# Performance work log

Measured on AMD Instinct MI355X. Metric: run time of the kernel, lower is better.

Reference implementation:

```python
import jax, jax.numpy as jnp
import numpy as np

NUM_EXPERTS = 8
TOP_K = 2
D_MODEL = 1024
D_MLP = 3584
BATCH, POS = 2, 2048


def setup_inputs() -> dict:
    key = jax.random.key(0)
    ks = jax.random.split(key, 5)
    scale = 0.02
    x = jax.random.normal(ks[0], (BATCH, POS, D_MODEL), dtype=jnp.float32)
    W_gate = jax.random.normal(ks[1], (NUM_EXPERTS, D_MODEL), dtype=jnp.float32) * scale
    W1 = jax.random.normal(ks[2], (NUM_EXPERTS, D_MLP, D_MODEL), dtype=jnp.float32) * scale
    W3 = jax.random.normal(ks[3], (NUM_EXPERTS, D_MLP, D_MODEL), dtype=jnp.float32) * scale
    W2 = jax.random.normal(ks[4], (NUM_EXPERTS, D_MODEL, D_MLP), dtype=jnp.float32) * scale
    return {"x": x, "W_gate": W_gate, "W1": W1, "W3": W3, "W2": W2}


def reference(x, W_gate, W1, W3, W2):
    batch, pos, d_model = x.shape
    xt = x.reshape(-1, d_model)                      # [T, d]
    T = xt.shape[0]

    # --- top-2 softmax gating ---
    gate_logits = xt @ W_gate.T                      # [T, E]
    weights = jax.nn.softmax(gate_logits.astype(jnp.float32), axis=-1)
    top_w, top_i = jax.lax.top_k(weights, TOP_K)     # [T, k]
    top_w = top_w / jnp.sum(top_w, axis=-1, keepdims=True)
    top_w = top_w.astype(gate_logits.dtype)

    # dense combine weights: zero for non-selected experts  [T, E]
    combine = jnp.zeros((T, NUM_EXPERTS), dtype=xt.dtype)
    combine = combine.at[jnp.arange(T)[:, None], top_i].set(top_w)

    # --- per-expert SwiGLU MLP, computed dense over all tokens ---
    h1 = jnp.einsum('td,efd->etf', xt, W1)           # [E, T, ffn]
    h3 = jnp.einsum('td,efd->etf', xt, W3)           # [E, T, ffn]
    h = jax.nn.silu(h1) * h3                         # [E, T, ffn]
    expert_out = jnp.einsum('etf,edf->etd', h, W2)   # [E, T, d]

    # --- weighted combine ---
    out = jnp.einsum('etd,te->td', expert_out, combine)  # [T, d]
    return out.reshape(batch, pos, d_model)
```

## Files before the change

kernel.cpp:

```cpp
#include <hip/hip_runtime.h>
#include <hip/hip_bf16.h>
#include <math.h>


#define NUM_EXPERTS 8
#define TOPK 2
#define D_MODEL 1024
#define D_MLP 3584
#define T_TOKENS 4096
#define NSLOT (T_TOKENS * TOPK)
#define SLOT_CAP 9216

#define BM 128
#define BN 128
#define BK 32
#define LDT 40

typedef __attribute__((ext_vector_type(8))) short bf16x8;
typedef __attribute__((ext_vector_type(4))) float f32x4;

#define WS_SMALL 147456
#define H_BYTES ((size_t)SLOT_CAP * D_MLP * 2)
#define XB_OFF (WS_SMALL + H_BYTES)
#define XB_BYTES ((size_t)T_TOKENS * D_MODEL * 2)
#define W1B_OFF (XB_OFF + XB_BYTES)
#define W13_BYTES ((size_t)NUM_EXPERTS * (size_t)D_MLP * D_MODEL * 2)
#define W3B_OFF (W1B_OFF + W13_BYTES)
#define WS_FULL (W3B_OFF + W13_BYTES)
#define WS_NEEDED_OLD (WS_SMALL + H_BYTES)

__device__ inline unsigned short f32_to_bf16(float f) {
  union { float f; unsigned int u; } v; v.f = f;
  unsigned int u = v.u;
  unsigned int r = (u + 0x7FFFu + ((u >> 16) & 1u)) >> 16;
  return (unsigned short)r;
}

__device__ inline bf16x8 pack8(float4 a, float4 b) {
  bf16x8 v;
  v[0] = (short)f32_to_bf16(a.x); v[1] = (short)f32_to_bf16(a.y);
  v[2] = (short)f32_to_bf16(a.z); v[3] = (short)f32_to_bf16(a.w);
  v[4] = (short)f32_to_bf16(b.x); v[5] = (short)f32_to_bf16(b.y);
  v[6] = (short)f32_to_bf16(b.z); v[7] = (short)f32_to_bf16(b.w);
  return v;
}

__device__ __forceinline__ void gload16(const void* g, void* l) {
  __builtin_amdgcn_global_load_lds(
      (__attribute__((address_space(1))) void*)g,
      (__attribute__((address_space(3))) void*)l, 16, 0, 0);
}

__global__ void zero_kernel(float4* __restrict__ p, int n4) {
  int i = blockIdx.x * blockDim.x + threadIdx.x;
  if (i < n4) p[i] = make_float4(0.f, 0.f, 0.f, 0.f);
}

__global__ __launch_bounds__(256) void cvt_kernel(const float* __restrict__ src,
                                                  unsigned short* __restrict__ dst,
                                                  int n8) {
  int i = blockIdx.x * blockDim.x + threadIdx.x;
  const int stride = gridDim.x * blockDim.x;
  for (; i < n8; i += stride) {
    const float4* s = (const float4*)(src + (size_t)i * 8);
    float4 a = s[0], b = s[1];
    *(bf16x8*)(dst + (size_t)i * 8) = pack8(a, b);
  }
}

__global__ __launch_bounds__(64) void gate_kernel(const float* __restrict__ x,
                            const float* __restrict__ Wg,
                            int* __restrict__ top_idx,
                            float* __restrict__ top_w) {
  const int t = blockIdx.x;
  const int lane = threadIdx.x;
  const float* xr = x + (size_t)t * D_MODEL;

  float xs[16];
#pragma unroll
  for (int i = 0; i < 16; ++i) xs[i] = xr[lane + i * 64];

  float logits[NUM_EXPERTS];
#pragma unroll
  for (int e = 0; e < NUM_EXPERTS; ++e) {
    const float* wr = Wg + (size_t)e * D_MODEL;
    float s = 0.f;
#pragma unroll
    for (int i = 0; i < 16; ++i) s += xs[i] * wr[lane + i * 64];
    for (int o = 32; o > 0; o >>= 1) s += __shfl_down(s, o);
    logits[e] = s;
  }

  if (lane == 0) {
    int i0 = 0;
#pragma unroll
    for (int e = 1; e < NUM_EXPERTS; ++e)
      if (logits[e] > logits[i0]) i0 = e;
    int i1 = -1;
#pragma unroll
    for (int e = 0; e < NUM_EXPERTS; ++e) {
      if (e == i0) continue;
      if (i1 < 0 || logits[e] > logits[i1]) i1 = e;
    }
    float w0 = 1.0f / (1.0f + expf(logits[i1] - logits[i0]));
    top_idx[2 * t] = i0; top_idx[2 * t + 1] = i1;
    top_w[2 * t] = w0;   top_w[2 * t + 1] = 1.0f - w0;
  }
}

__global__ __launch_bounds__(256) void route_kernel(int* __restrict__ top_idx,
                             const float* __restrict__ top_w,
                             int* __restrict__ hdr,
                             int* __restrict__ slot_token,
                             float* __restrict__ slot_weight) {
  __shared__ int cnt[NUM_EXPERTS];
  __shared__ int off[NUM_EXPERTS];
  __shared__ int cur[NUM_EXPERTS];
  const int tid = threadIdx.x;
  if (tid < NUM_EXPERTS) cnt[tid] = 0;
  __syncthreads();
  for (int k = tid; k < NSLOT; k += 256) atomicAdd(&cnt[top_idx[k]], 1);
  __syncthreads();
  if (tid == 0) {
    int o = 0;
    for (int e = 0; e < NUM_EXPERTS; ++e) {
      off[e] = o;
      int p = (cnt[e] + BM - 1) & ~(BM - 1);
      hdr[e] = cnt[e];
      hdr[8 + e] = o;
      hdr[16 + e] = p;
      o += p;
    }
  }
  __syncthreads();
  if (tid < NUM_EXPERTS) cur[tid] = off[tid];
  for (int i = tid; i < SLOT_CAP; i += 256) { slot_token[i] = 0; slot_weight[i] = 0.0f; }
  __syncthreads();
  for (int k = tid; k < NSLOT; k += 256) {
    int e = top_idx[k];
    int p = atomicAdd(&cur[e], 1);
    slot_token[p] = k >> 1;
    slot_weight[p] = top_w[k];
    top_idx[k] = p;
  }
}

__global__ __launch_bounds__(256) void gemm1_p(
    const unsigned short* __restrict__ Xb,
    const unsigned short* __restrict__ W1b,
    const unsigned short* __restrict__ W3b,
    const int* __restrict__ hdr,
    const int* __restrict__ slot_token,
    unsigned short* __restrict__ H) {
  const int e = blockIdx.z;
  const int pad_cnt = hdr[16 + e];
  const int m0 = blockIdx.y * BM;
  if (m0 >= pad_cnt) return;
  const int base = hdr[8 + e];
  const int n0 = blockIdx.x * BN;

  __shared__ unsigned short As[2][BM * BK];
  __shared__ unsigned short B1s[2][BN * BK];
  __shared__ unsigned short B3s[2][BN * BK];

  const int tid = threadIdx.x;
  const int lane = tid & 63;
  const int wave = tid >> 6;
  const int wm = (wave >> 1) * 64;
  const int wn = (wave & 1) * 64;
  const int l15 = lane & 15;
  const int quad = lane >> 4;

  const int r0 = tid >> 2;
  const int cc = (tid & 3) * 8;
  const int tokA0 = slot_token[base + m0 + r0];
  const int tokA1 = slot_token[base + m0 + 64 + r0];
  const unsigned short* gA0 = Xb + (size_t)tokA0 * D_MODEL + cc;
  const unsigned short* gA1 = Xb + (size_t)tokA1 * D_MODEL + cc;
  const unsigned short* gB1_0 = W1b + ((size_t)e * D_MLP + n0 + r0) * D_MODEL + cc;
  const unsigned short* gB1_1 = gB1_0 + (size_t)64 * D_MODEL;
  const unsigned short* gB3_0 = W3b + ((size_t)e * D_MLP + n0 + r0) * D_MODEL + cc;
  const unsigned short* gB3_1 = gB3_0 + (size_t)64 * D_MODEL;
  const int wb = wave * 512;

  const f32x4 fzero = {0.f, 0.f, 0.f, 0.f};
  f32x4 acc1[4][4], acc3[4][4];
#pragma unroll
  for (int i = 0; i < 4; ++i)
#pragma unroll
    for (int j = 0; j < 4; ++j) { acc1[i][j] = fzero; acc3[i][j] = fzero; }

#define NT1 (D_MODEL / BK)
  {
    gload16(gA0, &As[0][wb]);
    gload16(gA1, &As[0][2048 + wb]);
    gload16(gB1_0, &B1s[0][wb]);
    gload16(gB1_1, &B1s[0][2048 + wb]);
    gload16(gB3_0, &B3s[0][wb]);
    gload16(gB3_1, &B3s[0][2048 + wb]);
  }
  __syncthreads();

#pragma unroll
  for (int t = 0; t < NT1; ++t) {
    const int p = t & 1;
    if (t + 1 < NT1) {
      const int q = (t + 1) & 1;
      const int k1 = (t + 1) * BK;
      gload16(gA0 + k1, &As[q][wb]);
      gload16(gA1 + k1, &As[q][2048 + wb]);
      gload16(gB1_0 + k1, &B1s[q][wb]);
      gload16(gB1_1 + k1, &B1s[q][2048 + wb]);
      gload16(gB3_0 + k1, &B3s[q][wb]);
      gload16(gB3_1 + k1, &B3s[q][2048 + wb]);
    }
    bf16x8 af[4], b1f[4], b3f[4];
#pragma unroll
    for (int i = 0; i < 4; ++i)
      af[i] = *(const bf16x8*)(&As[p][(wm + i * 16 + l15) * BK + quad * 8]);
#pragma unroll
    for (int j = 0; j < 4; ++j) {
      b1f[j] = *(const bf16x8*)(&B1s[p][(wn + j * 16 + l15) * BK + quad * 8]);
      b3f[j] = *(const bf16x8*)(&B3s[p][(wn + j * 16 + l15) * BK + quad * 8]);
    }
#pragma unroll
    for (int i = 0; i < 4; ++i)
#pragma unroll
      for (int j = 0; j < 4; ++j) {
        acc1[i][j] = __builtin_amdgcn_mfma_f32_16x16x32_bf16(af[i], b1f[j], acc1[i][j], 0, 0, 0);
        acc3[i][j] = __builtin_amdgcn_mfma_f32_16x16x32_bf16(af[i], b3f[j], acc3[i][j], 0, 0, 0);
      }
    if (t + 1 < NT1) __syncthreads();
  }

  const size_t hbase = (size_t)(base + m0);
#pragma unroll
  for (int i = 0; i < 4; ++i) {
    const int mrow = wm + i * 16 + quad * 4;
#pragma unroll
    for (int r = 0; r < 4; ++r) {
      unsigned short* hrow = H + (hbase + mrow + r) * D_MLP + n0;
#pragma unroll
      for (int j = 0; j < 4; ++j) {
        float h1 = acc1[i][j][r];
        float h3 = acc3[i][j][r];
        float s = h1 / (1.0f + __expf(-h1));
        hrow[wn + j * 16 + l15] = f32_to_bf16(s * h3);
      }
    }
  }
}

__global__ __launch_bounds__(256) void gemm2_y(
    const unsigned short* __restrict__ H,
    const unsigned short* __restrict__ W2b,
    const int* __restrict__ hdr,
    float* __restrict__ Y) {
  const int e = blockIdx.z;
  const int pad_cnt = hdr[16 + e];
  const int m0 = blockIdx.y * BM;
  if (m0 >= pad_cnt) return;
  const int base = hdr[8 + e];
  const int n0 = blockIdx.x * BN;

  __shared__ unsigned short As[BM * LDT];
  __shared__ unsigned short Bs[BN * LDT];

  const int tid = threadIdx.x;
  const int lane = tid & 63;
  const int wave = tid >> 6;
  const int wm = (wave >> 1) * 64;
  const int wn = (wave & 1) * 64;
  const int l15 = lane & 15;
  const int quad = lane >> 4;

  const int sr = tid >> 1;
  const int sc = (tid & 1) * 16;
  const unsigned short* arow = H + (size_t)(base + m0 + sr) * D_MLP + sc;
  const unsigned short* brow = W2b + ((size_t)e * D_MODEL + n0 + sr) * D_MLP + sc;

  const f32x4 fzero = {0.f, 0.f, 0.f, 0.f};
  f32x4 acc[4][4];
#pragma unroll
  for (int i = 0; i < 4; ++i)
#pragma unroll
    for (int j = 0; j < 4; ++j) acc[i][j] = fzero;

  for (int k0 = 0; k0 < D_MLP; k0 += BK) {
    const uint4* ap = (const uint4*)(arow + k0);
    const uint4* bp = (const uint4*)(brow + k0);
    uint4 a0 = ap[0], a1 = ap[1];
    uint4 c0 = bp[0], c1 = bp[1];
    __syncthreads();
    *(uint4*)(&As[sr * LDT + sc]) = a0;
    *(uint4*)(&As[sr * LDT + sc + 8]) = a1;
    *(uint4*)(&Bs[sr * LDT + sc]) = c0;
    *(uint4*)(&Bs[sr * LDT + sc + 8]) = c1;
    __syncthreads();

    bf16x8 af[4], bf[4];
#pragma unroll
    for (int i = 0; i < 4; ++i)
      af[i] = *(const bf16x8*)(&As[(wm + i * 16 + l15) * LDT + quad * 8]);
#pragma unroll
    for (int j = 0; j < 4; ++j)
      bf[j] = *(const bf16x8*)(&Bs[(wn + j * 16 + l15) * LDT + quad * 8]);
#pragma unroll
    for (int i = 0; i < 4; ++i)
#pragma unroll
      for (int j = 0; j < 4; ++j)
        acc[i][j] = __builtin_amdgcn_mfma_f32_16x16x32_bf16(af[i], bf[j], acc[i][j], 0, 0, 0);
  }

#pragma unroll
  for (int i = 0; i < 4; ++i) {
    const int mrow = wm + i * 16 + quad * 4;
#pragma unroll
    for (int r = 0; r < 4; ++r) {
      float* yrow = Y + (size_t)(base + m0 + mrow + r) * D_MODEL + n0;
#pragma unroll
      for (int j = 0; j < 4; ++j)
        yrow[wn + j * 16 + l15] = acc[i][j][r];
    }
  }
}

__global__ __launch_bounds__(256) void combine_kernel(
    const float* __restrict__ Y,
    const int* __restrict__ slot_of,
    const float* __restrict__ top_w,
    float* __restrict__ out) {
  const int t = blockIdx.x;
  const int c = threadIdx.x;
  const int p0 = slot_of[2 * t], p1 = slot_of[2 * t + 1];
  const float w0 = top_w[2 * t], w1 = top_w[2 * t + 1];
  const float4 y0 = ((const float4*)(Y + (size_t)p0 * D_MODEL))[c];
  const float4 y1 = ((const float4*)(Y + (size_t)p1 * D_MODEL))[c];
  float4 o;
  o.x = w0 * y0.x + w1 * y1.x;
  o.y = w0 * y0.y + w1 * y1.y;
  o.z = w0 * y0.z + w1 * y1.z;
  o.w = w0 * y0.w + w1 * y1.w;
  ((float4*)(out + (size_t)t * D_MODEL))[c] = o;
}


__global__ __launch_bounds__(256) void gemm1_kernel(const float* __restrict__ x,
                             const float* __restrict__ W1,
                             const float* __restrict__ W3,
                             const int* __restrict__ hdr,
                             const int* __restrict__ slot_token,
                             unsigned short* __restrict__ H) {
  const int e = blockIdx.z;
  const int pad_cnt = hdr[16 + e];
  const int m0 = blockIdx.y * BM;
  if (m0 >= pad_cnt) return;
  const int base = hdr[8 + e];
  const int n0 = blockIdx.x * BN;

  __shared__ unsigned short As[BM * LDT];
  __shared__ unsigned short B1s[BN * LDT];
  __shared__ unsigned short B3s[BN * LDT];

  const int tid = threadIdx.x;
  const int lane = tid & 63;
  const int wave = tid >> 6;
  const int wm = (wave >> 1) * 64;
  const int wn = (wave & 1) * 64;
  const int l15 = lane & 15;
  const int quad = lane >> 4;

  const int sr = tid >> 1;
  const int sc = (tid & 1) * 16;
  const float* arow = x + (size_t)slot_token[base + m0 + sr] * D_MODEL + sc;
  const float* b1row = W1 + ((size_t)e * D_MLP + n0 + sr) * D_MODEL + sc;
  const float* b3row = W3 + ((size_t)e * D_MLP + n0 + sr) * D_MODEL + sc;

  const f32x4 fzero = {0.f, 0.f, 0.f, 0.f};
  f32x4 acc1[4][4], acc3[4][4];
#pragma unroll
  for (int i = 0; i < 4; ++i)
#pragma unroll
    for (int j = 0; j < 4; ++j) { acc1[i][j] = fzero; acc3[i][j] = fzero; }

  for (int k0 = 0; k0 < D_MODEL; k0 += BK) {
    const float4* ap = (const float4*)(arow + k0);
    const float4* b1p = (const float4*)(b1row + k0);
    const float4* b3p = (const float4*)(b3row + k0);
    float4 a0 = ap[0], a1 = ap[1], a2 = ap[2], a3 = ap[3];
    float4 c0 = b1p[0], c1 = b1p[1], c2 = b1p[2], c3 = b1p[3];
    float4 d0 = b3p[0], d1 = b3p[1], d2 = b3p[2], d3 = b3p[3];
    __syncthreads();
    *(bf16x8*)(&As[sr * LDT + sc]) = pack8(a0, a1);
    *(bf16x8*)(&As[sr * LDT + sc + 8]) = pack8(a2, a3);
    *(bf16x8*)(&B1s[sr * LDT + sc]) = pack8(c0, c1);
    *(bf16x8*)(&B1s[sr * LDT + sc + 8]) = pack8(c2, c3);
    *(bf16x8*)(&B3s[sr * LDT + sc]) = pack8(d0, d1);
    *(bf16x8*)(&B3s[sr * LDT + sc + 8]) = pack8(d2, d3);
    __syncthreads();

    bf16x8 a_frag[4], b1_frag[4], b3_frag[4];
#pragma unroll
    for (int i = 0; i < 4; ++i)
      a_frag[i] = *(const bf16x8*)(&As[(wm + i * 16 + l15) * LDT + quad * 8]);
#pragma unroll
    for (int j = 0; j < 4; ++j) {
      b1_frag[j] = *(const bf16x8*)(&B1s[(wn + j * 16 + l15) * LDT + quad * 8]);
      b3_frag[j] = *(const bf16x8*)(&B3s[(wn + j * 16 + l15) * LDT + quad * 8]);
    }
#pragma unroll
    for (int i = 0; i < 4; ++i)
#pragma unroll
      for (int j = 0; j < 4; ++j) {
        acc1[i][j] = __builtin_amdgcn_mfma_f32_16x16x32_bf16(a_frag[i], b1_frag[j], acc1[i][j], 0, 0, 0);
        acc3[i][j] = __builtin_amdgcn_mfma_f32_16x16x32_bf16(a_frag[i], b3_frag[j], acc3[i][j], 0, 0, 0);
      }
  }

  const size_t hbase = (size_t)(base + m0);
#pragma unroll
  for (int i = 0; i < 4; ++i) {
    const int mrow = wm + i * 16 + quad * 4;
#pragma unroll
    for (int r = 0; r < 4; ++r) {
      unsigned short* hrow = H + (hbase + mrow + r) * D_MLP + n0;
#pragma unroll
      for (int j = 0; j < 4; ++j) {
        float h1 = acc1[i][j][r];
        float h3 = acc3[i][j][r];
        float s = h1 / (1.0f + __expf(-h1));
        hrow[wn + j * 16 + l15] = f32_to_bf16(s * h3);
      }
    }
  }
}

__global__ __launch_bounds__(256) void gemm2_kernel(const unsigned short* __restrict__ H,
                             const float* __restrict__ W2,
                             const int* __restrict__ hdr,
                             const int* __restrict__ slot_token,
                             const float* __restrict__ slot_weight,
                             float* __restrict__ out) {
  const int e = blockIdx.z;
  const int pad_cnt = hdr[16 + e];
  const int m0 = blockIdx.y * BM;
  if (m0 >= pad_cnt) return;
  const int base = hdr[8 + e];
  const int n0 = blockIdx.x * BN;

  __shared__ unsigned short As[BM * LDT];
  __shared__ unsigned short Bs[BN * LDT];

  const int tid = threadIdx.x;
  const int lane = tid & 63;
  const int wave = tid >> 6;
  const int wm = (wave >> 1) * 64;
  const int wn = (wave & 1) * 64;
  const int l15 = lane & 15;
  const int quad = lane >> 4;

  const int sr = tid >> 1;
  const int sc = (tid & 1) * 16;
  const unsigned short* arow = H + (size_t)(base + m0 + sr) * D_MLP + sc;
  const float* brow = W2 + ((size_t)e * D_MODEL + n0 + sr) * D_MLP + sc;

  const f32x4 fzero = {0.f, 0.f, 0.f, 0.f};
  f32x4 acc[4][4];
#pragma unroll
  for (int i = 0; i < 4; ++i)
#pragma unroll
    for (int j = 0; j < 4; ++j) acc[i][j] = fzero;

  for (int k0 = 0; k0 < D_MLP; k0 += BK) {
    const uint4* ap = (const uint4*)(arow + k0);
    uint4 a0 = ap[0], a1 = ap[1];
    const float4* bp = (const float4*)(brow + k0);
    float4 c0 = bp[0], c1 = bp[1], c2 = bp[2], c3 = bp[3];
    __syncthreads();
    *(uint4*)(&As[sr * LDT + sc]) = a0;
    *(uint4*)(&As[sr * LDT + sc + 8]) = a1;
    *(bf16x8*)(&Bs[sr * LDT + sc]) = pack8(c0, c1);
    *(bf16x8*)(&Bs[sr * LDT + sc + 8]) = pack8(c2, c3);
    __syncthreads();

    bf16x8 a_frag[4], b_frag[4];
#pragma unroll
    for (int i = 0; i < 4; ++i)
      a_frag[i] = *(const bf16x8*)(&As[(wm + i * 16 + l15) * LDT + quad * 8]);
#pragma unroll
    for (int j = 0; j < 4; ++j)
      b_frag[j] = *(const bf16x8*)(&Bs[(wn + j * 16 + l15) * LDT + quad * 8]);
#pragma unroll
    for (int i = 0; i < 4; ++i)
#pragma unroll
      for (int j = 0; j < 4; ++j)
        acc[i][j] = __builtin_amdgcn_mfma_f32_16x16x32_bf16(a_frag[i], b_frag[j], acc[i][j], 0, 0, 0);
  }

#pragma unroll
  for (int i = 0; i < 4; ++i) {
    const int mrow = wm + i * 16 + quad * 4;
#pragma unroll
    for (int r = 0; r < 4; ++r) {
      const int srow = base + m0 + mrow + r;
      const float w = slot_weight[srow];
      if (w != 0.0f) {
        const int tok = slot_token[srow];
        float* orow = out + (size_t)tok * D_MODEL + n0;
#pragma unroll
        for (int j = 0; j < 4; ++j)
          atomicAdd(&orow[wn + j * 16 + l15], acc[i][j][r] * w);
      }
    }
  }
}

extern "C" void kernel_launch(void* const* d_in, const int* in_sizes, int n_in,
                              void* d_out, int out_size, void* d_ws, size_t ws_size,
                              hipStream_t stream) {
  const float* x  = (const float*)d_in[0];
  const float* Wg = (const float*)d_in[1];
  const float* W1 = (const float*)d_in[2];
  const float* W3 = (const float*)d_in[3];
  const float* W2 = (const float*)d_in[4];
  float* out = (float*)d_out;

  if (ws_size < WS_NEEDED_OLD) return;

  char* ws = (char*)d_ws;
  int*   top_idx     = (int*)(ws);
  float* top_w       = (float*)(ws + 32768);
  int*   hdr         = (int*)(ws + 65536);
  int*   slot_token  = (int*)(ws + 65792);
  float* slot_weight = (float*)(ws + 102656);
  unsigned short* H  = (unsigned short*)(ws + WS_SMALL);

  gate_kernel<<<T_TOKENS, 64, 0, stream>>>(x, Wg, top_idx, top_w);
  route_kernel<<<1, 256, 0, stream>>>(top_idx, top_w, hdr, slot_token, slot_weight);

  if (ws_size >= WS_FULL) {
    unsigned short* Xb  = (unsigned short*)(ws + XB_OFF);
    unsigned short* W1b = (unsigned short*)(ws + W1B_OFF);
    unsigned short* W3b = (unsigned short*)(ws + W3B_OFF);
    unsigned short* W2b = W1b;
    float* Y = (float*)(ws + W3B_OFF);

    cvt_kernel<<<2048, 256, 0, stream>>>(x, Xb, T_TOKENS * D_MODEL / 8);
    cvt_kernel<<<2048, 256, 0, stream>>>(W1, W1b, NUM_EXPERTS * D_MLP * D_MODEL / 8);
    cvt_kernel<<<2048, 256, 0, stream>>>(W3, W3b, NUM_EXPERTS * D_MLP * D_MODEL / 8);
    gemm1_p<<<dim3(D_MLP / BN, T_TOKENS / BM, NUM_EXPERTS), 256, 0, stream>>>(
        Xb, W1b, W3b, hdr, slot_token, H);
    cvt_kernel<<<2048, 256, 0, stream>>>(W2, W2b, NUM_EXPERTS * D_MODEL * D_MLP / 8);
    gemm2_y<<<dim3(D_MODEL / BN, T_TOKENS / BM, NUM_EXPERTS), 256, 0, stream>>>(
        H, W2b, hdr, Y);
    combine_kernel<<<T_TOKENS, 256, 0, stream>>>(Y, top_idx, top_w, out);
  } else {
    zero_kernel<<<(out_size / 4 + 255) / 256, 256, 0, stream>>>((float4*)d_out, out_size / 4);
    gemm1_kernel<<<dim3(D_MLP / BN, T_TOKENS / BM, NUM_EXPERTS), 256, 0, stream>>>(
        x, W1, W3, hdr, slot_token, H);
    gemm2_kernel<<<dim3(D_MODEL / BN, T_TOKENS / BM, NUM_EXPERTS), 256, 0, stream>>>(
        H, W2, hdr, slot_token, slot_weight, out);
  }
}
```

Measured before the change: 673.0 us.

## Double-buffer gemm2 LDS tiles with direct global-to-LDS async loads

Rewrites the second expert GEMM to use two LDS buffers and gload16 (presumably global-to-LDS direct loads, as gemm1_p already does) so the next K tile is fetched while MFMAs run on the current one. This drops the register staging and one of the two barriers per K step. The unpadded LDS layout (stride BK instead of LDT) may add bank conflicts on the fragment reads.

```diff
diff --git a/kernel.cpp b/kernel.cpp
--- a/kernel.cpp
+++ b/kernel.cpp
@@ -251,7 +251,7 @@
   }
 }
 
-__global__ __launch_bounds__(256) void gemm2_y(
+__global__ __launch_bounds__(256) void gemm2_p(
     const unsigned short* __restrict__ H,
     const unsigned short* __restrict__ W2b,
     const int* __restrict__ hdr,
@@ -263,8 +263,8 @@
   const int base = hdr[8 + e];
   const int n0 = blockIdx.x * BN;
 
-  __shared__ unsigned short As[BM * LDT];
-  __shared__ unsigned short Bs[BN * LDT];
+  __shared__ unsigned short As[2][BM * BK];
+  __shared__ unsigned short Bs[2][BN * BK];
 
   const int tid = threadIdx.x;
   const int lane = tid & 63;
@@ -274,10 +274,13 @@
   const int l15 = lane & 15;
   const int quad = lane >> 4;
 
-  const int sr = tid >> 1;
-  const int sc = (tid & 1) * 16;
-  const unsigned short* arow = H + (size_t)(base + m0 + sr) * D_MLP + sc;
-  const unsigned short* brow = W2b + ((size_t)e * D_MODEL + n0 + sr) * D_MLP + sc;
+  const int r0 = tid >> 2;
+  const int cc = (tid & 3) * 8;
+  const unsigned short* gA0 = H + (size_t)(base + m0 + r0) * D_MLP + cc;
+  const unsigned short* gA1 = gA0 + (size_t)64 * D_MLP;
+  const unsigned short* gB0 = W2b + ((size_t)e * D_MODEL + n0 + r0) * D_MLP + cc;
+  const unsigned short* gB1 = gB0 + (size_t)64 * D_MLP;
+  const int wb = wave * 512;
 
   const f32x4 fzero = {0.f, 0.f, 0.f, 0.f};
   f32x4 acc[4][4];
@@ -286,30 +289,37 @@
 #pragma unroll
     for (int j = 0; j < 4; ++j) acc[i][j] = fzero;
 
-  for (int k0 = 0; k0 < D_MLP; k0 += BK) {
-    const uint4* ap = (const uint4*)(arow + k0);
-    const uint4* bp = (const uint4*)(brow + k0);
-    uint4 a0 = ap[0], a1 = ap[1];
-    uint4 c0 = bp[0], c1 = bp[1];
-    __syncthreads();
-    *(uint4*)(&As[sr * LDT + sc]) = a0;
-    *(uint4*)(&As[sr * LDT + sc + 8]) = a1;
-    *(uint4*)(&Bs[sr * LDT + sc]) = c0;
-    *(uint4*)(&Bs[sr * LDT + sc + 8]) = c1;
-    __syncthreads();
-
+#define NT2 (D_MLP / BK)
+  gload16(gA0, &As[0][wb]);
+  gload16(gA1, &As[0][2048 + wb]);
+  gload16(gB0, &Bs[0][wb]);
+  gload16(gB1, &Bs[0][2048 + wb]);
+  __syncthreads();
+
+#pragma unroll 2
+  for (int t = 0; t < NT2; ++t) {
+    const int p = t & 1;
+    if (t + 1 < NT2) {
+      const int q = (t + 1) & 1;
+      const int k1 = (t + 1) * BK;
+      gload16(gA0 + k1, &As[q][wb]);
+      gload16(gA1 + k1, &As[q][2048 + wb]);
+      gload16(gB0 + k1, &Bs[q][wb]);
+      gload16(gB1 + k1, &Bs[q][2048 + wb]);
+    }
     bf16x8 af[4], bf[4];
 #pragma unroll
     for (int i = 0; i < 4; ++i)
-      af[i] = *(const bf16x8*)(&As[(wm + i * 16 + l15) * LDT + quad * 8]);
+      af[i] = *(const bf16x8*)(&As[p][(wm + i * 16 + l15) * BK + quad * 8]);
 #pragma unroll
     for (int j = 0; j < 4; ++j)
-      bf[j] = *(const bf16x8*)(&Bs[(wn + j * 16 + l15) * LDT + quad * 8]);
+      bf[j] = *(const bf16x8*)(&Bs[p][(wn + j * 16 + l15) * BK + quad * 8]);
 #pragma unroll
     for (int i = 0; i < 4; ++i)
 #pragma unroll
       for (int j = 0; j < 4; ++j)
         acc[i][j] = __builtin_amdgcn_mfma_f32_16x16x32_bf16(af[i], bf[j], acc[i][j], 0, 0, 0);
+    if (t + 1 < NT2) __syncthreads();
   }
 
 #pragma unroll
@@ -551,7 +561,7 @@
     gemm1_p<<<dim3(D_MLP / BN, T_TOKENS / BM, NUM_EXPERTS), 256, 0, stream>>>(
         Xb, W1b, W3b, hdr, slot_token, H);
     cvt_kernel<<<2048, 256, 0, stream>>>(W2, W2b, NUM_EXPERTS * D_MODEL * D_MLP / 8);
-    gemm2_y<<<dim3(D_MODEL / BN, T_TOKENS / BM, NUM_EXPERTS), 256, 0, stream>>>(
+    gemm2_p<<<dim3(D_MODEL / BN, T_TOKENS / BM, NUM_EXPERTS), 256, 0, stream>>>(
         H, W2b, hdr, Y);
     combine_kernel<<<T_TOKENS, 256, 0, stream>>>(Y, top_idx, top_w, out);
   } else {
```

Result: faster. 655.5 us (-2.6%).
